# Kernel tuning notes

Hardware: AMD Instinct MI355X
Metric: run time of the kernel (lower is better)

## Reference

```python
import jax, jax.numpy as jnp
import numpy as np

D_IN = 1024
D_OUT = 1024
N, S = 4, 2048

def setup_inputs() -> dict:
    key = jax.random.key(0)
    kv, kk, kq, k1, k2, k3 = jax.random.split(key, 6)
    return {
        "v": jax.random.normal(kv, (N, S, D_IN), dtype=jnp.float32),
        "k": jax.random.normal(kk, (N, S, D_IN), dtype=jnp.float32),
        "q": jax.random.normal(kq, (N, S, D_IN), dtype=jnp.float32),
        "WV": jax.random.normal(k1, (D_OUT, D_IN), dtype=jnp.float32),
        "WQ": jax.random.normal(k2, (D_OUT, D_IN), dtype=jnp.float32),
        "WK": jax.random.normal(k3, (D_OUT, D_IN), dtype=jnp.float32),
    }

def reference(v, k, q, WV, WQ, WK) -> jnp.ndarray:
    # projections: x @ W.T  -> [N, S, D_OUT]
    wv = jnp.einsum('nsw,ow->nso', v, WV)
    wk = jnp.einsum('nsw,ow->nso', k, WK)
    wq = jnp.einsum('nsw,ow->nso', q, WQ)
    # scores [N, Sq, Sk]; NOTE: softmax over axis=1 (query axis, matching torch dim=1),
    # then post-hoc division by input_shape[0] AFTER softmax (faithful to source).
    scores = jnp.einsum('nqo,nko->nqk', wq, wk)
    wqk = jax.nn.softmax(scores, axis=1) / jnp.float32(D_IN)
    return jnp.einsum('nqk,nko->nqo', wqk, wv)
```

## Files before the change

### kernel.cpp

```cpp
#include <hip/hip_runtime.h>
#include <math.h>


typedef _Float16 f16;
typedef _Float16 f16x8 __attribute__((ext_vector_type(8)));
typedef _Float16 f16x4 __attribute__((ext_vector_type(4)));
typedef float f32x4 __attribute__((ext_vector_type(4)));

enum StageMode { SM_PLANES2, SM_PLANES1 };
enum EpiMode   { EPI_F32, EPI_SPLIT, EPI_F16T };

#define GLL_PITCH 32

__device__ __forceinline__ void gll16(const f16* g, f16* l) {
    __builtin_amdgcn_global_load_lds(
        (const __attribute__((address_space(1))) void*)g,
        (__attribute__((address_space(3))) void*)l, 16, 0, 0);
}

__device__ __forceinline__ void stage_gll_plane(const f16* __restrict__ gplane,
                                                f16* __restrict__ lds,
                                                long rowBase, int ld, int k0,
                                                int wave, int lane)
{
#pragma unroll
    for (int i = 0; i < 2; i++) {
        int slotBase = (wave * 2 + i) * 64;
        int t = slotBase + lane;
        int r = t >> 2;
        int c = (t & 3) ^ ((r >> 1) & 3);
        const f16* g = gplane + (rowBase + r) * (long)ld + k0 + c * 8;
        gll16(g, lds + (long)slotBase * 8);
    }
}

__device__ __forceinline__ int frag_off_gll(int row, int g) {
    return row * GLL_PITCH + ((g ^ ((row >> 1) & 3)) << 3);
}

template<StageMode SA, StageMode SB, EpiMode EP, int GROUPM, bool STATS>
__global__ __launch_bounds__(256, 4)
void mfma_gemm(const f16* __restrict__ Ahi, const f16* __restrict__ Alo,
               const f16* __restrict__ Bhi, const f16* __restrict__ Blo,
               float* __restrict__ pmOut, float* __restrict__ psOut,
               void* __restrict__ C0, void* __restrict__ C1,
               int M, int Nc, int K, int lda, int ldb, int ldc,
               long batchA, long batchB, long batchC,
               float epiScale, int tsShift)
{
    constexpr bool TRIPLE = (SA == SM_PLANES2);
    constexpr int PLANE_SZ = 128 * GLL_PITCH;

    int bx, by;
    if constexpr (GROUPM > 0) {
        int gx = gridDim.x;
        int lin = blockIdx.y * gx + blockIdx.x;
        int nig = GROUPM * gx;
        int gid = lin / nig;
        int rem = lin - gid * nig;
        by = gid * GROUPM + (rem % GROUPM);
        bx = rem / GROUPM;
    } else {
        bx = blockIdx.x;
        by = blockIdx.y;
    }
    const int n0 = bx * 128;
    const int m0 = by * 128;
    const long z = blockIdx.z;

    const long aOfs = z * batchA, bOfs = z * batchB, cOfs = z * batchC;

    __shared__ __align__(16) f16 As_hi[PLANE_SZ];
    __shared__ __align__(16) f16 Bs_hi[PLANE_SZ];
    __shared__ __align__(16) f16 As_lo[TRIPLE ? PLANE_SZ : 8];
    __shared__ __align__(16) f16 Bs_lo[TRIPLE ? PLANE_SZ : 8];

    const int tid  = threadIdx.x;
    const int lane = tid & 63;
    const int wave = tid >> 6;
    const int wr = (wave >> 1) * 64;
    const int wc = (wave & 1) * 64;
    const int fm = lane & 15;
    const int fg = lane >> 4;

    f32x4 acc[4][4];
#pragma unroll
    for (int i = 0; i < 4; i++)
#pragma unroll
        for (int j = 0; j < 4; j++) acc[i][j] = (f32x4){0.f, 0.f, 0.f, 0.f};

    int roA[4], roB[4];
#pragma unroll
    for (int i = 0; i < 4; i++) {
        roA[i] = frag_off_gll(wr + i * 16 + fm, fg);
        roB[i] = frag_off_gll(wc + i * 16 + fm, fg);
    }

    for (int k0 = 0; k0 < K; k0 += 32) {
        stage_gll_plane(Ahi + aOfs, As_hi, m0, lda, k0, wave, lane);
        stage_gll_plane(Bhi + bOfs, Bs_hi, n0, ldb, k0, wave, lane);
        if constexpr (TRIPLE) {
            stage_gll_plane(Alo + aOfs, As_lo, m0, lda, k0, wave, lane);
            stage_gll_plane(Blo + bOfs, Bs_lo, n0, ldb, k0, wave, lane);
        }
        __syncthreads();

        f16x8 ah[4], bh[4], al[4], bl[4];
#pragma unroll
        for (int i = 0; i < 4; i++) {
            ah[i] = *(const f16x8*)&As_hi[roA[i]];
            bh[i] = *(const f16x8*)&Bs_hi[roB[i]];
            if constexpr (TRIPLE) {
                al[i] = *(const f16x8*)&As_lo[roA[i]];
                bl[i] = *(const f16x8*)&Bs_lo[roB[i]];
            }
        }
#pragma unroll
        for (int i = 0; i < 4; i++) {
#pragma unroll
            for (int j = 0; j < 4; j++) {
                acc[i][j] = __builtin_amdgcn_mfma_f32_16x16x32_f16(ah[i], bh[j], acc[i][j], 0, 0, 0);
                if constexpr (TRIPLE) {
                    acc[i][j] = __builtin_amdgcn_mfma_f32_16x16x32_f16(ah[i], bl[j], acc[i][j], 0, 0, 0);
                    acc[i][j] = __builtin_amdgcn_mfma_f32_16x16x32_f16(al[i], bh[j], acc[i][j], 0, 0, 0);
                }
            }
        }
        __syncthreads();
    }

    const int cr = fg * 4;
    const int cn = fm;
#pragma unroll
    for (int i = 0; i < 4; i++) {
#pragma unroll
        for (int j = 0; j < 4; j++) {
#pragma unroll
            for (int r = 0; r < 4; r++) {
                long mg = m0 + wr + i * 16 + cr + r;
                long ng = n0 + wc + j * 16 + cn;
                float val = acc[i][j][r] * epiScale;
                if constexpr (EP == EPI_F32) {
                    ((float*)C0)[cOfs + mg * ldc + ng] = val;
                } else if constexpr (EP == EPI_SPLIT) {
                    f16 h = (f16)val;
                    ((f16*)C0)[cOfs + mg * ldc + ng] = h;
                    ((f16*)C1)[cOfs + mg * ldc + ng] = (f16)(val - (float)h);
                } else {
                    long TS = 1L << tsShift;
                    long nb = mg >> tsShift;
                    long s  = mg & (TS - 1);
                    long addr = nb * ((long)Nc << tsShift) + ng * TS + s;
                    ((f16*)C0)[addr] = (f16)val;
                }
            }
        }
    }
}

template<EpiMode EP, bool STATS, bool XCDMAP, bool DUAL>
__global__ __launch_bounds__(512, 2)
void big_gemm(const f16* __restrict__ Ahi, const f16* __restrict__ Alo,
              const f16* __restrict__ Bhi, const f16* __restrict__ Blo,
              const f16* __restrict__ A2hi, const f16* __restrict__ A2lo,
              const f16* __restrict__ B2hi, const f16* __restrict__ B2lo,
              float* __restrict__ pmOut, float* __restrict__ psOut,
              void* __restrict__ C0, void* __restrict__ C1,
              void* __restrict__ C20, void* __restrict__ C21,
              int M, int Nc, int K, int lda, int ldb, int ldc,
              long batchA, long batchB, long batchC, int msplitTiles)
{
    constexpr int PLANE = 256 * GLL_PITCH;

    __shared__ __align__(16) f16 As_hi[2][PLANE];
    __shared__ __align__(16) f16 As_lo[2][PLANE];
    __shared__ __align__(16) f16 Bs_hi[2][PLANE];
    __shared__ __align__(16) f16 Bs_lo[2][PLANE];

    const int tid  = threadIdx.x;
    const int lane = tid & 63;
    const int wave = tid >> 6;
    const int rw   = wave >> 2;
    const int cw   = wave & 3;
    const int wrM  = rw * 128;
    const int wrN  = cw * 64;
    const int fm   = lane & 15;
    const int fg   = lane >> 4;

    int bxn, byn, zn;
    if constexpr (XCDMAP) {
        const int Lid = (int)(blockIdx.z * 64 + blockIdx.y * 8 + blockIdx.x);
        const int xcd = Lid & 7;
        const int sct = Lid >> 3;
        bxn = sct & 7;
        const int idxp = xcd * 4 + (sct >> 3);
        byn = idxp & 7;
        zn  = idxp >> 3;
    } else {
        bxn = blockIdx.x;
        byn = blockIdx.y;
        zn  = blockIdx.z;
    }

    const f16* pAhi = Ahi; const f16* pAlo = Alo;
    const f16* pBhi = Bhi; const f16* pBlo = Blo;
    void* pC0 = C0; void* pC1 = C1;
    int mTile = byn;
    if constexpr (DUAL) {
        if (byn >= msplitTiles) {
            pAhi = A2hi; pAlo = A2lo; pBhi = B2hi; pBlo = B2lo;
            pC0 = C20; pC1 = C21;
            mTile = byn - msplitTiles;
        }
    }

    const int n0 = bxn * 256;
    const int m0 = mTile * 256;
    const long z = zn;
    const long aOfs = z * batchA, bOfs = z * batchB, cOfs = z * batchC;

    int slotBase[2], srcA[2], srcB[2];
#pragma unroll
    for (int i = 0; i < 2; i++) {
        int sb = (wave * 2 + i) * 64;
        int t  = sb + lane;
        int r  = t >> 2;
        int c  = (t & 3) ^ ((r >> 1) & 3);
        slotBase[i] = sb * 8;
        srcA[i] = (m0 + r) * lda + c * 8;
        srcB[i] = (n0 + r) * ldb + c * 8;
    }

#define SC_STAGE(buf, k0) do {                                               \
    _Pragma("unroll")                                                        \
    for (int s_ = 0; s_ < 2; s_++) {                                         \
        gll16(pAhi + aOfs + srcA[s_] + (k0), &As_hi[buf][slotBase[s_]]);     \
        gll16(pAlo + aOfs + srcA[s_] + (k0), &As_lo[buf][slotBase[s_]]);     \
        gll16(pBhi + bOfs + srcB[s_] + (k0), &Bs_hi[buf][slotBase[s_]]);     \
        gll16(pBlo + bOfs + srcB[s_] + (k0), &Bs_lo[buf][slotBase[s_]]);     \
    } } while (0)

    f32x4 acc[8][4];
#pragma unroll
    for (int i = 0; i < 8; i++)
#pragma unroll
        for (int j = 0; j < 4; j++) acc[i][j] = (f32x4){0.f, 0.f, 0.f, 0.f};

    int roA[8], roB[4];
#pragma unroll
    for (int i = 0; i < 8; i++) roA[i] = frag_off_gll(wrM + i * 16 + fm, fg);
#pragma unroll
    for (int j = 0; j < 4; j++) roB[j] = frag_off_gll(wrN + j * 16 + fm, fg);

    const int NT = K >> 5;
    SC_STAGE(0, 0);
    SC_STAGE(1, 32);

    for (int t = 0; t < NT; t++) {
        const int cur = t & 1;
        if (t == 0) {
            asm volatile("s_waitcnt vmcnt(8)" ::: "memory");
        } else {
            asm volatile("s_waitcnt vmcnt(0)" ::: "memory");
        }
        __builtin_amdgcn_sched_barrier(0);
        __builtin_amdgcn_s_barrier();
        __builtin_amdgcn_sched_barrier(0);

        if (t >= 1 && t + 1 < NT) SC_STAGE(cur ^ 1, (t + 1) * 32);
        __builtin_amdgcn_sched_barrier(0);

        f16x8 bh[4], a0h[4];
#pragma unroll
        for (int j = 0; j < 4; j++) bh[j] = *(const f16x8*)&Bs_hi[cur][roB[j]];
#pragma unroll
        for (int i = 0; i < 4; i++) a0h[i] = *(const f16x8*)&As_hi[cur][roA[i]];
        __builtin_amdgcn_sched_barrier(0);
        f16x8 bl[4], a0l[4];
#pragma unroll
        for (int j = 0; j < 4; j++) bl[j] = *(const f16x8*)&Bs_lo[cur][roB[j]];
#pragma unroll
        for (int i = 0; i < 4; i++) a0l[i] = *(const f16x8*)&As_lo[cur][roA[i]];
        __builtin_amdgcn_sched_barrier(0);

        __builtin_amdgcn_s_setprio(1);
#pragma unroll
        for (int i = 0; i < 4; i++)
#pragma unroll
            for (int j = 0; j < 4; j++)
                acc[i][j] = __builtin_amdgcn_mfma_f32_16x16x32_f16(a0h[i], bh[j], acc[i][j], 0, 0, 0);
        __builtin_amdgcn_s_setprio(0);
        __builtin_amdgcn_sched_barrier(0);

        f16x8 a1h[4], a1l[4];
#pragma unroll
        for (int i = 0; i < 4; i++) {
            a1h[i] = *(const f16x8*)&As_hi[cur][roA[4 + i]];
            a1l[i] = *(const f16x8*)&As_lo[cur][roA[4 + i]];
        }
        __builtin_amdgcn_sched_barrier(0);

        __builtin_amdgcn_s_setprio(1);
#pragma unroll
        for (int i = 0; i < 4; i++)
#pragma unroll
            for (int j = 0; j < 4; j++)
                acc[i][j] = __builtin_amdgcn_mfma_f32_16x16x32_f16(a0h[i], bl[j], acc[i][j], 0, 0, 0);
#pragma unroll
        for (int i = 0; i < 4; i++)
#pragma unroll
            for (int j = 0; j < 4; j++)
                acc[i][j] = __builtin_amdgcn_mfma_f32_16x16x32_f16(a0l[i], bh[j], acc[i][j], 0, 0, 0);
        __builtin_amdgcn_s_setprio(0);
        __builtin_amdgcn_sched_barrier(0);

        __builtin_amdgcn_s_setprio(1);
#pragma unroll
        for (int i = 0; i < 4; i++)
#pragma unroll
            for (int j = 0; j < 4; j++)
                acc[4 + i][j] = __builtin_amdgcn_mfma_f32_16x16x32_f16(a1h[i], bh[j], acc[4 + i][j], 0, 0, 0);
#pragma unroll
        for (int i = 0; i < 4; i++)
#pragma unroll
            for (int j = 0; j < 4; j++)
                acc[4 + i][j] = __builtin_amdgcn_mfma_f32_16x16x32_f16(a1h[i], bl[j], acc[4 + i][j], 0, 0, 0);
#pragma unroll
        for (int i = 0; i < 4; i++)
#pragma unroll
            for (int j = 0; j < 4; j++)
                acc[4 + i][j] = __builtin_amdgcn_mfma_f32_16x16x32_f16(a1l[i], bh[j], acc[4 + i][j], 0, 0, 0);
        __builtin_amdgcn_s_setprio(0);
    }
#undef SC_STAGE

    const int cr = fg * 4;
#pragma unroll
    for (int i = 0; i < 8; i++) {
#pragma unroll
        for (int j = 0; j < 4; j++) {
#pragma unroll
            for (int r = 0; r < 4; r++) {
                long mg = m0 + wrM + i * 16 + cr + r;
                long ng = n0 + wrN + j * 16 + fm;
                float val = acc[i][j][r];
                if constexpr (EP == EPI_F32) {
                    ((float*)pC0)[cOfs + mg * (long)ldc + ng] = val;
                } else {
                    f16 h = (f16)val;
                    ((f16*)pC0)[cOfs + mg * (long)ldc + ng] = h;
                    ((f16*)pC1)[cOfs + mg * (long)ldc + ng] = (f16)(val - (float)h);
                }
            }
        }
    }

    if constexpr (STATS) {
        __shared__ float stM[2][256];
        __shared__ float stS[2][256];
#pragma unroll
        for (int j = 0; j < 4; j++) {
            float mj = -3.402823466e38f;
#pragma unroll
            for (int i = 0; i < 8; i++)
#pragma unroll
                for (int r = 0; r < 4; r++) mj = fmaxf(mj, acc[i][j][r]);
            float sj = 0.f;
#pragma unroll
            for (int i = 0; i < 8; i++)
#pragma unroll
                for (int r = 0; r < 4; r++) sj += __expf(acc[i][j][r] - mj);
#pragma unroll
            for (int mask = 16; mask <= 32; mask <<= 1) {
                float mo = __shfl_xor(mj, mask, 64);
                float so = __shfl_xor(sj, mask, 64);
                float mn = fmaxf(mj, mo);
                sj = sj * __expf(mj - mn) + so * __expf(mo - mn);
                mj = mn;
            }
            if (fg == 0) {
                stM[rw][wrN + j * 16 + fm] = mj;
                stS[rw][wrN + j * 16 + fm] = sj;
            }
        }
        __syncthreads();
        if (tid < 256) {
            float ma = stM[0][tid], mb = stM[1][tid];
            float Mc = fmaxf(ma, mb);
            float Sv = stS[0][tid] * __expf(ma - Mc) + stS[1][tid] * __expf(mb - Mc);
            long o = ((long)z * (M >> 8) + byn) * (long)Nc + (long)bxn * 256 + tid;
            pmOut[o] = Mc;
            psOut[o] = Sv;
        }
    }
}

__global__ __launch_bounds__(256)
void split_all_kernel(const float* __restrict__ q, const float* __restrict__ k,
                      const float* __restrict__ v, const float* __restrict__ WQ,
                      const float* __restrict__ WK, const float* __restrict__ WV,
                      f16* __restrict__ ws, long NSD, long DD)
{
    const long QB = NSD / 2048;
    const long WB = DD / 2048;
    const long b = blockIdx.x;
    f16* Wb = ws + 5 * NSD;

    const float* src;
    f16* hi;
    f16* lo = nullptr;
    long base;
    if (b < QB)               { src = q;  base = b * 2048;                 hi = ws;           lo = ws + NSD;   }
    else if (b < 2 * QB)      { src = k;  base = (b - QB) * 2048;          hi = ws + 2 * NSD; lo = ws + 3 * NSD; }
    else if (b < 3 * QB)      { src = v;  base = (b - 2 * QB) * 2048;      hi = ws + 4 * NSD; }
    else if (b < 3 * QB + WB) { src = WQ; base = (b - 3 * QB) * 2048;      hi = Wb;           lo = Wb + DD;    }
    else if (b < 3 * QB + 2 * WB) { src = WK; base = (b - 3 * QB - WB) * 2048; hi = Wb + 2 * DD; lo = Wb + 3 * DD; }
    else                      { src = WV; base = (b - 3 * QB - 2 * WB) * 2048; hi = Wb + 4 * DD; }

    long i = base + (long)threadIdx.x * 8;
    float4 x0 = *(const float4*)&src[i];
    float4 x1 = *(const float4*)&src[i + 4];
    float xs[8] = {x0.x, x0.y, x0.z, x0.w, x1.x, x1.y, x1.z, x1.w};
    f16x8 h, l;
#pragma unroll
    for (int e = 0; e < 8; e++) {
        f16 hh = (f16)xs[e];
        h[e] = hh;
        l[e] = (f16)(xs[e] - (float)hh);
    }
    *(f16x8*)&hi[i] = h;
    if (lo) *(f16x8*)&lo[i] = l;
}

__global__ __launch_bounds__(256)
void pmat_kernel(const float* __restrict__ Sc, const float* __restrict__ pm,
                 const float* __restrict__ ps, f16* __restrict__ Phi, int S)
{
    const int n = blockIdx.z;
    const int kk = blockIdx.x * 1024 + threadIdx.x * 4;
    const float* Sn = Sc + (long)n * S * S;
    f16* ph = Phi + (long)n * S * S;

    float M4[4], R4[4];
#pragma unroll
    for (int c = 0; c < 4; c++) {
        const int col = kk + c;
        float pmv[8];
        float M = -INFINITY;
#pragma unroll
        for (int i = 0; i < 8; i++) {
            pmv[i] = pm[((long)n * 8 + i) * S + col];
            M = fmaxf(M, pmv[i]);
        }
        float Ssum = 0.f;
#pragma unroll
        for (int i = 0; i < 8; i++)
            Ssum += ps[((long)n * 8 + i) * S + col] * __expf(pmv[i] - M);
        M4[c] = M;
        R4[c] = 1.0f / Ssum;
    }

    const int q0 = blockIdx.y * 32;
    for (int qi = 0; qi < 32; qi++) {
        long idx = (long)(q0 + qi) * S + kk;
        float4 x = *(const float4*)&Sn[idx];
        f16x4 p;
        p[0] = (f16)(__expf(x.x - M4[0]) * R4[0]);
        p[1] = (f16)(__expf(x.y - M4[1]) * R4[1]);
        p[2] = (f16)(__expf(x.z - M4[2]) * R4[2]);
        p[3] = (f16)(__expf(x.w - M4[3]) * R4[3]);
        *(f16x4*)&ph[idx] = p;
    }
}

extern "C" void kernel_launch(void* const* d_in, const int* in_sizes, int n_in,
                              void* d_out, int out_size, void* d_ws, size_t ws_size,
                              hipStream_t stream)
{
    const float* v  = (const float*)d_in[0];
    const float* k  = (const float*)d_in[1];
    const float* q  = (const float*)d_in[2];
    const float* WV = (const float*)d_in[3];
    const float* WQ = (const float*)d_in[4];
    const float* WK = (const float*)d_in[5];
    float* out = (float*)d_out;

    const int N = 4, S = 2048, D = 1024;
    const long NSD = (long)N * S * D;
    const long DD  = (long)D * D;

    f16* ws = (f16*)d_ws;
    f16* q_hi = ws;
    f16* q_lo = ws + NSD;
    f16* k_hi = ws + 2 * NSD;
    f16* k_lo = ws + 3 * NSD;
    f16* v_hi = ws + 4 * NSD;
    f16* Wb   = ws + 5 * NSD;
    f16* WQ_hi = Wb,          *WQ_lo = Wb + DD;
    f16* WK_hi = Wb + 2 * DD, *WK_lo = Wb + 3 * DD;
    f16* WV_hi = Wb + 4 * DD;
    f16* wq_hi = ws + 5 * NSD + 5 * DD;
    f16* wq_lo = wq_hi + NSD;
    f16* wk_hi = wq_hi + 2 * NSD;
    f16* wk_lo = wq_hi + 3 * NSD;
    f16* wvT_hi = ws;
    float* Sc   = (float*)(ws + NSD);
    f16* P_hi   = wq_hi;
    float* pm    = (float*)(ws + 9 * NSD + 5 * DD);
    float* ps    = pm + (long)N * 8 * S;

    dim3 blk(256);

    {
        long nblocks = 3 * (NSD / 2048) + 3 * (DD / 2048);
        split_all_kernel<<<dim3((unsigned)nblocks), blk, 0, stream>>>(
            q, k, v, WQ, WK, WV, ws, NSD, DD);
    }

    {
        dim3 g(D / 256, (2 * N * S) / 256, 1);
        big_gemm<EPI_SPLIT, false, false, true><<<g, dim3(512), 0, stream>>>(
            q_hi, q_lo, WQ_hi, WQ_lo,
            k_hi, k_lo, WK_hi, WK_lo,
            nullptr, nullptr,
            wq_hi, wq_lo, wk_hi, wk_lo,
            2 * N * S, D, D, D, D, D, 0, 0, 0, (N * S) / 256 );
    }
    {
        dim3 g(D / 128, (N * S) / 128, 1);
        mfma_gemm<SM_PLANES1, SM_PLANES1, EPI_F16T, 4, false><<<g, blk, 0, stream>>>(
            v_hi, nullptr, WV_hi, nullptr, nullptr, nullptr, wvT_hi, nullptr,
            N * S, D, D, D, D, 0, 0, 0, 0, 1.0f, 11 );
    }
    {
        dim3 g(S / 256, S / 256, N);
        big_gemm<EPI_F32, true, true, false><<<g, dim3(512), 0, stream>>>(
            wq_hi, wq_lo, wk_hi, wk_lo,
            nullptr, nullptr, nullptr, nullptr,
            pm, ps, Sc, nullptr, nullptr, nullptr,
            S, S, D, D, D, S, (long)S * D, (long)S * D, (long)S * S, 1 << 30);
    }
    {
        dim3 g(S / 1024, S / 32, N);
        pmat_kernel<<<g, blk, 0, stream>>>(Sc, pm, ps, P_hi, S);
    }
    {
        dim3 g(D / 128, S / 128, N);
        mfma_gemm<SM_PLANES1, SM_PLANES1, EPI_F32, 4, false><<<g, blk, 0, stream>>>(
            P_hi, nullptr, wvT_hi, nullptr, nullptr, nullptr, out, nullptr,
            S, D, S, S, S, D, (long)S * S, (long)S * D, (long)S * D, 1.0f / (float)D, 0);
    }
}
```

Measured before the change: 438.7 us.

## Route single-plane GEMMs through the double-buffered 256x256 big_gemm kernel

Removes the simple 128x128 single-buffered mfma_gemm kernel. The V projection and the final P·V GEMM now run on big_gemm, which gains a TRIPLE template flag so it can skip the low-precision planes, plus the F16T transposed epilogue and an epilogue scale. It also adds an XCD-aware block remapping mode for the dual Q/K projection. The aim is to get larger tiles, double-buffered async loads and more data reuse for the fp16-only GEMMs. The cost is fewer blocks per launch (for example 128 for the P·V GEMM), which may lower occupancy, and the remap assumes a fixed grid shape.

```diff
diff --git a/kernel.cpp b/kernel.cpp
--- a/kernel.cpp
+++ b/kernel.cpp
@@ -7,8 +7,7 @@
 typedef _Float16 f16x4 __attribute__((ext_vector_type(4)));
 typedef float f32x4 __attribute__((ext_vector_type(4)));
 
-enum StageMode { SM_PLANES2, SM_PLANES1 };
-enum EpiMode   { EPI_F32, EPI_SPLIT, EPI_F16T };
+enum EpiMode { EPI_F32, EPI_SPLIT, EPI_F16T };
 
 #define GLL_PITCH 32
 
@@ -18,147 +17,11 @@
         (__attribute__((address_space(3))) void*)l, 16, 0, 0);
 }
 
-__device__ __forceinline__ void stage_gll_plane(const f16* __restrict__ gplane,
-                                                f16* __restrict__ lds,
-                                                long rowBase, int ld, int k0,
-                                                int wave, int lane)
-{
-#pragma unroll
-    for (int i = 0; i < 2; i++) {
-        int slotBase = (wave * 2 + i) * 64;
-        int t = slotBase + lane;
-        int r = t >> 2;
-        int c = (t & 3) ^ ((r >> 1) & 3);
-        const f16* g = gplane + (rowBase + r) * (long)ld + k0 + c * 8;
-        gll16(g, lds + (long)slotBase * 8);
-    }
-}
-
 __device__ __forceinline__ int frag_off_gll(int row, int g) {
     return row * GLL_PITCH + ((g ^ ((row >> 1) & 3)) << 3);
 }
 
-template<StageMode SA, StageMode SB, EpiMode EP, int GROUPM, bool STATS>
-__global__ __launch_bounds__(256, 4)
-void mfma_gemm(const f16* __restrict__ Ahi, const f16* __restrict__ Alo,
-               const f16* __restrict__ Bhi, const f16* __restrict__ Blo,
-               float* __restrict__ pmOut, float* __restrict__ psOut,
-               void* __restrict__ C0, void* __restrict__ C1,
-               int M, int Nc, int K, int lda, int ldb, int ldc,
-               long batchA, long batchB, long batchC,
-               float epiScale, int tsShift)
-{
-    constexpr bool TRIPLE = (SA == SM_PLANES2);
-    constexpr int PLANE_SZ = 128 * GLL_PITCH;
-
-    int bx, by;
-    if constexpr (GROUPM > 0) {
-        int gx = gridDim.x;
-        int lin = blockIdx.y * gx + blockIdx.x;
-        int nig = GROUPM * gx;
-        int gid = lin / nig;
-        int rem = lin - gid * nig;
-        by = gid * GROUPM + (rem % GROUPM);
-        bx = rem / GROUPM;
-    } else {
-        bx = blockIdx.x;
-        by = blockIdx.y;
-    }
-    const int n0 = bx * 128;
-    const int m0 = by * 128;
-    const long z = blockIdx.z;
-
-    const long aOfs = z * batchA, bOfs = z * batchB, cOfs = z * batchC;
-
-    __shared__ __align__(16) f16 As_hi[PLANE_SZ];
-    __shared__ __align__(16) f16 Bs_hi[PLANE_SZ];
-    __shared__ __align__(16) f16 As_lo[TRIPLE ? PLANE_SZ : 8];
-    __shared__ __align__(16) f16 Bs_lo[TRIPLE ? PLANE_SZ : 8];
-
-    const int tid  = threadIdx.x;
-    const int lane = tid & 63;
-    const int wave = tid >> 6;
-    const int wr = (wave >> 1) * 64;
-    const int wc = (wave & 1) * 64;
-    const int fm = lane & 15;
-    const int fg = lane >> 4;
-
-    f32x4 acc[4][4];
-#pragma unroll
-    for (int i = 0; i < 4; i++)
-#pragma unroll
-        for (int j = 0; j < 4; j++) acc[i][j] = (f32x4){0.f, 0.f, 0.f, 0.f};
-
-    int roA[4], roB[4];
-#pragma unroll
-    for (int i = 0; i < 4; i++) {
-        roA[i] = frag_off_gll(wr + i * 16 + fm, fg);
-        roB[i] = frag_off_gll(wc + i * 16 + fm, fg);
-    }
-
-    for (int k0 = 0; k0 < K; k0 += 32) {
-        stage_gll_plane(Ahi + aOfs, As_hi, m0, lda, k0, wave, lane);
-        stage_gll_plane(Bhi + bOfs, Bs_hi, n0, ldb, k0, wave, lane);
-        if constexpr (TRIPLE) {
-            stage_gll_plane(Alo + aOfs, As_lo, m0, lda, k0, wave, lane);
-            stage_gll_plane(Blo + bOfs, Bs_lo, n0, ldb, k0, wave, lane);
-        }
-        __syncthreads();
-
-        f16x8 ah[4], bh[4], al[4], bl[4];
-#pragma unroll
-        for (int i = 0; i < 4; i++) {
-            ah[i] = *(const f16x8*)&As_hi[roA[i]];
-            bh[i] = *(const f16x8*)&Bs_hi[roB[i]];
-            if constexpr (TRIPLE) {
-                al[i] = *(const f16x8*)&As_lo[roA[i]];
-                bl[i] = *(const f16x8*)&Bs_lo[roB[i]];
-            }
-        }
-#pragma unroll
-        for (int i = 0; i < 4; i++) {
-#pragma unroll
-            for (int j = 0; j < 4; j++) {
-                acc[i][j] = __builtin_amdgcn_mfma_f32_16x16x32_f16(ah[i], bh[j], acc[i][j], 0, 0, 0);
-                if constexpr (TRIPLE) {
-                    acc[i][j] = __builtin_amdgcn_mfma_f32_16x16x32_f16(ah[i], bl[j], acc[i][j], 0, 0, 0);
-                    acc[i][j] = __builtin_amdgcn_mfma_f32_16x16x32_f16(al[i], bh[j], acc[i][j], 0, 0, 0);
-                }
-            }
-        }
-        __syncthreads();
-    }
-
-    const int cr = fg * 4;
-    const int cn = fm;
-#pragma unroll
-    for (int i = 0; i < 4; i++) {
-#pragma unroll
-        for (int j = 0; j < 4; j++) {
-#pragma unroll
-            for (int r = 0; r < 4; r++) {
-                long mg = m0 + wr + i * 16 + cr + r;
-                long ng = n0 + wc + j * 16 + cn;
-                float val = acc[i][j][r] * epiScale;
-                if constexpr (EP == EPI_F32) {
-                    ((float*)C0)[cOfs + mg * ldc + ng] = val;
-                } else if constexpr (EP == EPI_SPLIT) {
-                    f16 h = (f16)val;
-                    ((f16*)C0)[cOfs + mg * ldc + ng] = h;
-                    ((f16*)C1)[cOfs + mg * ldc + ng] = (f16)(val - (float)h);
-                } else {
-                    long TS = 1L << tsShift;
-                    long nb = mg >> tsShift;
-                    long s  = mg & (TS - 1);
-                    long addr = nb * ((long)Nc << tsShift) + ng * TS + s;
-                    ((f16*)C0)[addr] = (f16)val;
-                }
-            }
-        }
-    }
-}
-
-template<EpiMode EP, bool STATS, bool XCDMAP, bool DUAL>
+template<EpiMode EP, bool STATS, int XCDMODE, bool DUAL, bool TRIPLE>
 __global__ __launch_bounds__(512, 2)
 void big_gemm(const f16* __restrict__ Ahi, const f16* __restrict__ Alo,
               const f16* __restrict__ Bhi, const f16* __restrict__ Blo,
@@ -168,14 +31,15 @@
               void* __restrict__ C0, void* __restrict__ C1,
               void* __restrict__ C20, void* __restrict__ C21,
               int M, int Nc, int K, int lda, int ldb, int ldc,
-              long batchA, long batchB, long batchC, int msplitTiles)
+              long batchA, long batchB, long batchC, int msplitTiles,
+              float epiScale, int tsShift)
 {
     constexpr int PLANE = 256 * GLL_PITCH;
 
     __shared__ __align__(16) f16 As_hi[2][PLANE];
-    __shared__ __align__(16) f16 As_lo[2][PLANE];
     __shared__ __align__(16) f16 Bs_hi[2][PLANE];
-    __shared__ __align__(16) f16 Bs_lo[2][PLANE];
+    __shared__ __align__(16) f16 As_lo[2][TRIPLE ? PLANE : 8];
+    __shared__ __align__(16) f16 Bs_lo[2][TRIPLE ? PLANE : 8];
 
     const int tid  = threadIdx.x;
     const int lane = tid & 63;
@@ -188,7 +52,7 @@
     const int fg   = lane >> 4;
 
     int bxn, byn, zn;
-    if constexpr (XCDMAP) {
+    if constexpr (XCDMODE == 1) {
         const int Lid = (int)(blockIdx.z * 64 + blockIdx.y * 8 + blockIdx.x);
         const int xcd = Lid & 7;
         const int sct = Lid >> 3;
@@ -196,6 +60,13 @@
         const int idxp = xcd * 4 + (sct >> 3);
         byn = idxp & 7;
         zn  = idxp >> 3;
+    } else if constexpr (XCDMODE == 2) {
+        const int Lid = (int)(blockIdx.y * 4 + blockIdx.x);
+        const int xcd = Lid & 7;
+        const int sct = Lid >> 3;
+        bxn = sct & 3;
+        byn = xcd * 8 + (sct >> 2);
+        zn  = 0;
     } else {
         bxn = blockIdx.x;
         byn = blockIdx.y;
@@ -231,13 +102,15 @@
         srcB[i] = (n0 + r) * ldb + c * 8;
     }
 
-#define SC_STAGE(buf, k0) do {                                               \
-    _Pragma("unroll")                                                        \
-    for (int s_ = 0; s_ < 2; s_++) {                                         \
-        gll16(pAhi + aOfs + srcA[s_] + (k0), &As_hi[buf][slotBase[s_]]);     \
-        gll16(pAlo + aOfs + srcA[s_] + (k0), &As_lo[buf][slotBase[s_]]);     \
-        gll16(pBhi + bOfs + srcB[s_] + (k0), &Bs_hi[buf][slotBase[s_]]);     \
-        gll16(pBlo + bOfs + srcB[s_] + (k0), &Bs_lo[buf][slotBase[s_]]);     \
+#define SC_STAGE(buf, k0) do {                                                   \
+    _Pragma("unroll")                                                            \
+    for (int s_ = 0; s_ < 2; s_++) {                                             \
+        gll16(pAhi + aOfs + srcA[s_] + (k0), &As_hi[buf][slotBase[s_]]);         \
+        gll16(pBhi + bOfs + srcB[s_] + (k0), &Bs_hi[buf][slotBase[s_]]);         \
+        if constexpr (TRIPLE) {                                                  \
+            gll16(pAlo + aOfs + srcA[s_] + (k0), &As_lo[buf][slotBase[s_]]);     \
+            gll16(pBlo + bOfs + srcB[s_] + (k0), &Bs_lo[buf][slotBase[s_]]);     \
+        }                                                                        \
     } } while (0)
 
     f32x4 acc[8][4];
@@ -259,7 +132,8 @@
     for (int t = 0; t < NT; t++) {
         const int cur = t & 1;
         if (t == 0) {
-            asm volatile("s_waitcnt vmcnt(8)" ::: "memory");
+            if constexpr (TRIPLE) asm volatile("s_waitcnt vmcnt(8)" ::: "memory");
+            else                  asm volatile("s_waitcnt vmcnt(4)" ::: "memory");
         } else {
             asm volatile("s_waitcnt vmcnt(0)" ::: "memory");
         }
@@ -277,11 +151,13 @@
         for (int i = 0; i < 4; i++) a0h[i] = *(const f16x8*)&As_hi[cur][roA[i]];
         __builtin_amdgcn_sched_barrier(0);
         f16x8 bl[4], a0l[4];
-#pragma unroll
-        for (int j = 0; j < 4; j++) bl[j] = *(const f16x8*)&Bs_lo[cur][roB[j]];
-#pragma unroll
-        for (int i = 0; i < 4; i++) a0l[i] = *(const f16x8*)&As_lo[cur][roA[i]];
-        __builtin_amdgcn_sched_barrier(0);
+        if constexpr (TRIPLE) {
+#pragma unroll
+            for (int j = 0; j < 4; j++) bl[j] = *(const f16x8*)&Bs_lo[cur][roB[j]];
+#pragma unroll
+            for (int i = 0; i < 4; i++) a0l[i] = *(const f16x8*)&As_lo[cur][roA[i]];
+            __builtin_amdgcn_sched_barrier(0);
+        }
 
         __builtin_amdgcn_s_setprio(1);
 #pragma unroll
@@ -296,23 +172,25 @@
 #pragma unroll
         for (int i = 0; i < 4; i++) {
             a1h[i] = *(const f16x8*)&As_hi[cur][roA[4 + i]];
-            a1l[i] = *(const f16x8*)&As_lo[cur][roA[4 + i]];
-        }
-        __builtin_amdgcn_sched_barrier(0);
-
-        __builtin_amdgcn_s_setprio(1);
-#pragma unroll
-        for (int i = 0; i < 4; i++)
-#pragma unroll
-            for (int j = 0; j < 4; j++)
-                acc[i][j] = __builtin_amdgcn_mfma_f32_16x16x32_f16(a0h[i], bl[j], acc[i][j], 0, 0, 0);
-#pragma unroll
-        for (int i = 0; i < 4; i++)
-#pragma unroll
-            for (int j = 0; j < 4; j++)
-                acc[i][j] = __builtin_amdgcn_mfma_f32_16x16x32_f16(a0l[i], bh[j], acc[i][j], 0, 0, 0);
-        __builtin_amdgcn_s_setprio(0);
-        __builtin_amdgcn_sched_barrier(0);
+            if constexpr (TRIPLE) a1l[i] = *(const f16x8*)&As_lo[cur][roA[4 + i]];
+        }
+        __builtin_amdgcn_sched_barrier(0);
+
+        if constexpr (TRIPLE) {
+            __builtin_amdgcn_s_setprio(1);
+#pragma unroll
+            for (int i = 0; i < 4; i++)
+#pragma unroll
+                for (int j = 0; j < 4; j++)
+                    acc[i][j] = __builtin_amdgcn_mfma_f32_16x16x32_f16(a0h[i], bl[j], acc[i][j], 0, 0, 0);
+#pragma unroll
+            for (int i = 0; i < 4; i++)
+#pragma unroll
+                for (int j = 0; j < 4; j++)
+                    acc[i][j] = __builtin_amdgcn_mfma_f32_16x16x32_f16(a0l[i], bh[j], acc[i][j], 0, 0, 0);
+            __builtin_amdgcn_s_setprio(0);
+            __builtin_amdgcn_sched_barrier(0);
+        }
 
         __builtin_amdgcn_s_setprio(1);
 #pragma unroll
@@ -320,16 +198,18 @@
 #pragma unroll
             for (int j = 0; j < 4; j++)
                 acc[4 + i][j] = __builtin_amdgcn_mfma_f32_16x16x32_f16(a1h[i], bh[j], acc[4 + i][j], 0, 0, 0);
-#pragma unroll
-        for (int i = 0; i < 4; i++)
-#pragma unroll
-            for (int j = 0; j < 4; j++)
-                acc[4 + i][j] = __builtin_amdgcn_mfma_f32_16x16x32_f16(a1h[i], bl[j], acc[4 + i][j], 0, 0, 0);
-#pragma unroll
-        for (int i = 0; i < 4; i++)
-#pragma unroll
-            for (int j = 0; j < 4; j++)
-                acc[4 + i][j] = __builtin_amdgcn_mfma_f32_16x16x32_f16(a1l[i], bh[j], acc[4 + i][j], 0, 0, 0);
+        if constexpr (TRIPLE) {
+#pragma unroll
+            for (int i = 0; i < 4; i++)
+#pragma unroll
+                for (int j = 0; j < 4; j++)
+                    acc[4 + i][j] = __builtin_amdgcn_mfma_f32_16x16x32_f16(a1h[i], bl[j], acc[4 + i][j], 0, 0, 0);
+#pragma unroll
+            for (int i = 0; i < 4; i++)
+#pragma unroll
+                for (int j = 0; j < 4; j++)
+                    acc[4 + i][j] = __builtin_amdgcn_mfma_f32_16x16x32_f16(a1l[i], bh[j], acc[4 + i][j], 0, 0, 0);
+        }
         __builtin_amdgcn_s_setprio(0);
     }
 #undef SC_STAGE
@@ -343,13 +223,19 @@
             for (int r = 0; r < 4; r++) {
                 long mg = m0 + wrM + i * 16 + cr + r;
                 long ng = n0 + wrN + j * 16 + fm;
-                float val = acc[i][j][r];
+                float val = acc[i][j][r] * epiScale;
                 if constexpr (EP == EPI_F32) {
                     ((float*)pC0)[cOfs + mg * (long)ldc + ng] = val;
-                } else {
+                } else if constexpr (EP == EPI_SPLIT) {
                     f16 h = (f16)val;
                     ((f16*)pC0)[cOfs + mg * (long)ldc + ng] = h;
                     ((f16*)pC1)[cOfs + mg * (long)ldc + ng] = (f16)(val - (float)h);
+                } else {
+                    long TS = 1L << tsShift;
+                    long nb = mg >> tsShift;
+                    long s  = mg & (TS - 1);
+                    long addr = nb * ((long)Nc << tsShift) + ng * TS + s;
+                    ((f16*)pC0)[addr] = (f16)val;
                 }
             }
         }
@@ -519,35 +405,42 @@
 
     {
         dim3 g(D / 256, (2 * N * S) / 256, 1);
-        big_gemm<EPI_SPLIT, false, false, true><<<g, dim3(512), 0, stream>>>(
+        big_gemm<EPI_SPLIT, false, 2, true, true><<<g, dim3(512), 0, stream>>>(
             q_hi, q_lo, WQ_hi, WQ_lo,
             k_hi, k_lo, WK_hi, WK_lo,
             nullptr, nullptr,
             wq_hi, wq_lo, wk_hi, wk_lo,
-            2 * N * S, D, D, D, D, D, 0, 0, 0, (N * S) / 256 );
-    }
-    {
-        dim3 g(D / 128, (N * S) / 128, 1);
-        mfma_gemm<SM_PLANES1, SM_PLANES1, EPI_F16T, 4, false><<<g, blk, 0, stream>>>(
-            v_hi, nullptr, WV_hi, nullptr, nullptr, nullptr, wvT_hi, nullptr,
-            N * S, D, D, D, D, 0, 0, 0, 0, 1.0f, 11 );
+            2 * N * S, D, D, D, D, D, 0, 0, 0, (N * S) / 256 , 1.0f, 0);
+    }
+    {
+        dim3 g(D / 256, (N * S) / 256, 1);
+        big_gemm<EPI_F16T, false, 0, false, false><<<g, dim3(512), 0, stream>>>(
+            v_hi, nullptr, WV_hi, nullptr,
+            nullptr, nullptr, nullptr, nullptr,
+            nullptr, nullptr,
+            wvT_hi, nullptr, nullptr, nullptr,
+            N * S, D, D, D, D, 0, 0, 0, 0, 1 << 30, 1.0f, 11 );
     }
     {
         dim3 g(S / 256, S / 256, N);
-        big_gemm<EPI_F32, true, true, false><<<g, dim3(512), 0, stream>>>(
+        big_gemm<EPI_F32, true, 1, false, true><<<g, dim3(512), 0, stream>>>(
             wq_hi, wq_lo, wk_hi, wk_lo,
             nullptr, nullptr, nullptr, nullptr,
             pm, ps, Sc, nullptr, nullptr, nullptr,
-            S, S, D, D, D, S, (long)S * D, (long)S * D, (long)S * S, 1 << 30);
+            S, S, D, D, D, S, (long)S * D, (long)S * D, (long)S * S, 1 << 30, 1.0f, 0);
     }
     {
         dim3 g(S / 1024, S / 32, N);
         pmat_kernel<<<g, blk, 0, stream>>>(Sc, pm, ps, P_hi, S);
     }
     {
-        dim3 g(D / 128, S / 128, N);
-        mfma_gemm<SM_PLANES1, SM_PLANES1, EPI_F32, 4, false><<<g, blk, 0, stream>>>(
-            P_hi, nullptr, wvT_hi, nullptr, nullptr, nullptr, out, nullptr,
-            S, D, S, S, S, D, (long)S * S, (long)S * D, (long)S * D, 1.0f / (float)D, 0);
-    }
-}
+        dim3 g(D / 256, S / 256, N);
+        big_gemm<EPI_F32, false, 0, false, false><<<g, dim3(512), 0, stream>>>(
+            P_hi, nullptr, wvT_hi, nullptr,
+            nullptr, nullptr, nullptr, nullptr,
+            nullptr, nullptr,
+            out, nullptr, nullptr, nullptr,
+            S, D, S, S, S, D, (long)S * S, (long)S * D, (long)S * D, 1 << 30,
+            1.0f / (float)D, 0);
+    }
+}
```

New measurement: 496.7 us. +13.2%, slower.

## Fuse tile-local exp into scores GEMM epilogue, store f16 scores, remap projection blocks

Applied to the files above, without the earlier changes.

The scores GEMM now finishes its per-tile column statistics first, then writes exp(score - tileMax) as f16 instead of raw f32 scores. The softmax kernel becomes a cheap in-place rescale of those f16 values by a per-column weight built from the tile and global maxima. This halves the score-matrix traffic and moves the exponentials into the GEMM epilogue. It also adds an XCD-aware block remap for the fused Q/K projection GEMM and a template switch to drop the lo-plane loads and MFMAs (all current launches keep them), at the cost of an extra f16 rounding of the unnormalised probabilities.

```diff
diff --git a/kernel.cpp b/kernel.cpp
--- a/kernel.cpp
+++ b/kernel.cpp
@@ -158,7 +158,7 @@
     }
 }
 
-template<EpiMode EP, bool STATS, bool XCDMAP, bool DUAL>
+template<EpiMode EP, bool STATS, int XCDMODE, bool DUAL, bool TRIPLE>
 __global__ __launch_bounds__(512, 2)
 void big_gemm(const f16* __restrict__ Ahi, const f16* __restrict__ Alo,
               const f16* __restrict__ Bhi, const f16* __restrict__ Blo,
@@ -173,9 +173,9 @@
     constexpr int PLANE = 256 * GLL_PITCH;
 
     __shared__ __align__(16) f16 As_hi[2][PLANE];
-    __shared__ __align__(16) f16 As_lo[2][PLANE];
     __shared__ __align__(16) f16 Bs_hi[2][PLANE];
-    __shared__ __align__(16) f16 Bs_lo[2][PLANE];
+    __shared__ __align__(16) f16 As_lo[2][TRIPLE ? PLANE : 8];
+    __shared__ __align__(16) f16 Bs_lo[2][TRIPLE ? PLANE : 8];
 
     const int tid  = threadIdx.x;
     const int lane = tid & 63;
@@ -188,7 +188,7 @@
     const int fg   = lane >> 4;
 
     int bxn, byn, zn;
-    if constexpr (XCDMAP) {
+    if constexpr (XCDMODE == 1) {
         const int Lid = (int)(blockIdx.z * 64 + blockIdx.y * 8 + blockIdx.x);
         const int xcd = Lid & 7;
         const int sct = Lid >> 3;
@@ -196,6 +196,13 @@
         const int idxp = xcd * 4 + (sct >> 3);
         byn = idxp & 7;
         zn  = idxp >> 3;
+    } else if constexpr (XCDMODE == 2) {
+        const int Lid = (int)(blockIdx.y * 4 + blockIdx.x);
+        const int xcd = Lid & 7;
+        const int sct = Lid >> 3;
+        bxn = sct & 3;
+        byn = xcd * 8 + (sct >> 2);
+        zn  = 0;
     } else {
         bxn = blockIdx.x;
         byn = blockIdx.y;
@@ -231,13 +238,15 @@
         srcB[i] = (n0 + r) * ldb + c * 8;
     }
 
-#define SC_STAGE(buf, k0) do {                                               \
-    _Pragma("unroll")                                                        \
-    for (int s_ = 0; s_ < 2; s_++) {                                         \
-        gll16(pAhi + aOfs + srcA[s_] + (k0), &As_hi[buf][slotBase[s_]]);     \
-        gll16(pAlo + aOfs + srcA[s_] + (k0), &As_lo[buf][slotBase[s_]]);     \
-        gll16(pBhi + bOfs + srcB[s_] + (k0), &Bs_hi[buf][slotBase[s_]]);     \
-        gll16(pBlo + bOfs + srcB[s_] + (k0), &Bs_lo[buf][slotBase[s_]]);     \
+#define SC_STAGE(buf, k0) do {                                                   \
+    _Pragma("unroll")                                                            \
+    for (int s_ = 0; s_ < 2; s_++) {                                             \
+        gll16(pAhi + aOfs + srcA[s_] + (k0), &As_hi[buf][slotBase[s_]]);         \
+        gll16(pBhi + bOfs + srcB[s_] + (k0), &Bs_hi[buf][slotBase[s_]]);         \
+        if constexpr (TRIPLE) {                                                  \
+            gll16(pAlo + aOfs + srcA[s_] + (k0), &As_lo[buf][slotBase[s_]]);     \
+            gll16(pBlo + bOfs + srcB[s_] + (k0), &Bs_lo[buf][slotBase[s_]]);     \
+        }                                                                        \
     } } while (0)
 
     f32x4 acc[8][4];
@@ -259,7 +268,8 @@
     for (int t = 0; t < NT; t++) {
         const int cur = t & 1;
         if (t == 0) {
-            asm volatile("s_waitcnt vmcnt(8)" ::: "memory");
+            if constexpr (TRIPLE) asm volatile("s_waitcnt vmcnt(8)" ::: "memory");
+            else                  asm volatile("s_waitcnt vmcnt(4)" ::: "memory");
         } else {
             asm volatile("s_waitcnt vmcnt(0)" ::: "memory");
         }
@@ -277,11 +287,13 @@
         for (int i = 0; i < 4; i++) a0h[i] = *(const f16x8*)&As_hi[cur][roA[i]];
         __builtin_amdgcn_sched_barrier(0);
         f16x8 bl[4], a0l[4];
-#pragma unroll
-        for (int j = 0; j < 4; j++) bl[j] = *(const f16x8*)&Bs_lo[cur][roB[j]];
-#pragma unroll
-        for (int i = 0; i < 4; i++) a0l[i] = *(const f16x8*)&As_lo[cur][roA[i]];
-        __builtin_amdgcn_sched_barrier(0);
+        if constexpr (TRIPLE) {
+#pragma unroll
+            for (int j = 0; j < 4; j++) bl[j] = *(const f16x8*)&Bs_lo[cur][roB[j]];
+#pragma unroll
+            for (int i = 0; i < 4; i++) a0l[i] = *(const f16x8*)&As_lo[cur][roA[i]];
+            __builtin_amdgcn_sched_barrier(0);
+        }
 
         __builtin_amdgcn_s_setprio(1);
 #pragma unroll
@@ -296,23 +308,25 @@
 #pragma unroll
         for (int i = 0; i < 4; i++) {
             a1h[i] = *(const f16x8*)&As_hi[cur][roA[4 + i]];
-            a1l[i] = *(const f16x8*)&As_lo[cur][roA[4 + i]];
+            if constexpr (TRIPLE) a1l[i] = *(const f16x8*)&As_lo[cur][roA[4 + i]];
         }
         __builtin_amdgcn_sched_barrier(0);
 
-        __builtin_amdgcn_s_setprio(1);
-#pragma unroll
-        for (int i = 0; i < 4; i++)
-#pragma unroll
-            for (int j = 0; j < 4; j++)
-                acc[i][j] = __builtin_amdgcn_mfma_f32_16x16x32_f16(a0h[i], bl[j], acc[i][j], 0, 0, 0);
-#pragma unroll
-        for (int i = 0; i < 4; i++)
-#pragma unroll
-            for (int j = 0; j < 4; j++)
-                acc[i][j] = __builtin_amdgcn_mfma_f32_16x16x32_f16(a0l[i], bh[j], acc[i][j], 0, 0, 0);
-        __builtin_amdgcn_s_setprio(0);
-        __builtin_amdgcn_sched_barrier(0);
+        if constexpr (TRIPLE) {
+            __builtin_amdgcn_s_setprio(1);
+#pragma unroll
+            for (int i = 0; i < 4; i++)
+#pragma unroll
+                for (int j = 0; j < 4; j++)
+                    acc[i][j] = __builtin_amdgcn_mfma_f32_16x16x32_f16(a0h[i], bl[j], acc[i][j], 0, 0, 0);
+#pragma unroll
+            for (int i = 0; i < 4; i++)
+#pragma unroll
+                for (int j = 0; j < 4; j++)
+                    acc[i][j] = __builtin_amdgcn_mfma_f32_16x16x32_f16(a0l[i], bh[j], acc[i][j], 0, 0, 0);
+            __builtin_amdgcn_s_setprio(0);
+            __builtin_amdgcn_sched_barrier(0);
+        }
 
         __builtin_amdgcn_s_setprio(1);
 #pragma unroll
@@ -320,40 +334,23 @@
 #pragma unroll
             for (int j = 0; j < 4; j++)
                 acc[4 + i][j] = __builtin_amdgcn_mfma_f32_16x16x32_f16(a1h[i], bh[j], acc[4 + i][j], 0, 0, 0);
-#pragma unroll
-        for (int i = 0; i < 4; i++)
-#pragma unroll
-            for (int j = 0; j < 4; j++)
-                acc[4 + i][j] = __builtin_amdgcn_mfma_f32_16x16x32_f16(a1h[i], bl[j], acc[4 + i][j], 0, 0, 0);
-#pragma unroll
-        for (int i = 0; i < 4; i++)
-#pragma unroll
-            for (int j = 0; j < 4; j++)
-                acc[4 + i][j] = __builtin_amdgcn_mfma_f32_16x16x32_f16(a1l[i], bh[j], acc[4 + i][j], 0, 0, 0);
+        if constexpr (TRIPLE) {
+#pragma unroll
+            for (int i = 0; i < 4; i++)
+#pragma unroll
+                for (int j = 0; j < 4; j++)
+                    acc[4 + i][j] = __builtin_amdgcn_mfma_f32_16x16x32_f16(a1h[i], bl[j], acc[4 + i][j], 0, 0, 0);
+#pragma unroll
+            for (int i = 0; i < 4; i++)
+#pragma unroll
+                for (int j = 0; j < 4; j++)
+                    acc[4 + i][j] = __builtin_amdgcn_mfma_f32_16x16x32_f16(a1l[i], bh[j], acc[4 + i][j], 0, 0, 0);
+        }
         __builtin_amdgcn_s_setprio(0);
     }
 #undef SC_STAGE
 
     const int cr = fg * 4;
-#pragma unroll
-    for (int i = 0; i < 8; i++) {
-#pragma unroll
-        for (int j = 0; j < 4; j++) {
-#pragma unroll
-            for (int r = 0; r < 4; r++) {
-                long mg = m0 + wrM + i * 16 + cr + r;
-                long ng = n0 + wrN + j * 16 + fm;
-                float val = acc[i][j][r];
-                if constexpr (EP == EPI_F32) {
-                    ((float*)pC0)[cOfs + mg * (long)ldc + ng] = val;
-                } else {
-                    f16 h = (f16)val;
-                    ((f16*)pC0)[cOfs + mg * (long)ldc + ng] = h;
-                    ((f16*)pC1)[cOfs + mg * (long)ldc + ng] = (f16)(val - (float)h);
-                }
-            }
-        }
-    }
 
     if constexpr (STATS) {
         __shared__ float stM[2][256];
@@ -391,6 +388,43 @@
             long o = ((long)z * (M >> 8) + byn) * (long)Nc + (long)bxn * 256 + tid;
             pmOut[o] = Mc;
             psOut[o] = Sv;
+            stM[0][tid] = Mc;
+        }
+        __syncthreads();
+
+#pragma unroll
+        for (int j = 0; j < 4; j++) {
+            const float Mc = stM[0][wrN + j * 16 + fm];
+#pragma unroll
+            for (int i = 0; i < 8; i++) {
+#pragma unroll
+                for (int r = 0; r < 4; r++) {
+                    long mg = m0 + wrM + i * 16 + cr + r;
+                    long ng = n0 + wrN + j * 16 + fm;
+                    ((f16*)pC0)[cOfs + mg * (long)ldc + ng] =
+                        (f16)__expf(acc[i][j][r] - Mc);
+                }
+            }
+        }
+    } else {
+#pragma unroll
+        for (int i = 0; i < 8; i++) {
+#pragma unroll
+            for (int j = 0; j < 4; j++) {
+#pragma unroll
+                for (int r = 0; r < 4; r++) {
+                    long mg = m0 + wrM + i * 16 + cr + r;
+                    long ng = n0 + wrN + j * 16 + fm;
+                    float val = acc[i][j][r];
+                    if constexpr (EP == EPI_F32) {
+                        ((float*)pC0)[cOfs + mg * (long)ldc + ng] = val;
+                    } else {
+                        f16 h = (f16)val;
+                        ((f16*)pC0)[cOfs + mg * (long)ldc + ng] = h;
+                        ((f16*)pC1)[cOfs + mg * (long)ldc + ng] = (f16)(val - (float)h);
+                    }
+                }
+            }
         }
     }
 }
@@ -433,15 +467,16 @@
 }
 
 __global__ __launch_bounds__(256)
-void pmat_kernel(const float* __restrict__ Sc, const float* __restrict__ pm,
-                 const float* __restrict__ ps, f16* __restrict__ Phi, int S)
+void pmat_kernel(f16* __restrict__ P, const float* __restrict__ pm,
+                 const float* __restrict__ ps, int S)
 {
     const int n = blockIdx.z;
     const int kk = blockIdx.x * 1024 + threadIdx.x * 4;
-    const float* Sn = Sc + (long)n * S * S;
-    f16* ph = Phi + (long)n * S * S;
-
-    float M4[4], R4[4];
+    const int q0 = blockIdx.y * 32;
+    const int tile = q0 >> 8;
+    f16* Pn = P + (long)n * S * S;
+
+    float w4[4];
 #pragma unroll
     for (int c = 0; c < 4; c++) {
         const int col = kk + c;
@@ -456,20 +491,16 @@
 #pragma unroll
         for (int i = 0; i < 8; i++)
             Ssum += ps[((long)n * 8 + i) * S + col] * __expf(pmv[i] - M);
-        M4[c] = M;
-        R4[c] = 1.0f / Ssum;
-    }
-
-    const int q0 = blockIdx.y * 32;
+        w4[c] = __expf(pmv[tile] - M) / Ssum;
+    }
+
     for (int qi = 0; qi < 32; qi++) {
         long idx = (long)(q0 + qi) * S + kk;
-        float4 x = *(const float4*)&Sn[idx];
+        f16x4 ph = *(const f16x4*)&Pn[idx];
         f16x4 p;
-        p[0] = (f16)(__expf(x.x - M4[0]) * R4[0]);
-        p[1] = (f16)(__expf(x.y - M4[1]) * R4[1]);
-        p[2] = (f16)(__expf(x.z - M4[2]) * R4[2]);
-        p[3] = (f16)(__expf(x.w - M4[3]) * R4[3]);
-        *(f16x4*)&ph[idx] = p;
+#pragma unroll
+        for (int e = 0; e < 4; e++) p[e] = (f16)((float)ph[e] * w4[e]);
+        *(f16x4*)&Pn[idx] = p;
     }
 }
 
@@ -504,8 +535,7 @@
     f16* wk_hi = wq_hi + 2 * NSD;
     f16* wk_lo = wq_hi + 3 * NSD;
     f16* wvT_hi = ws;
-    float* Sc   = (float*)(ws + NSD);
-    f16* P_hi   = wq_hi;
+    f16* Sc16   = ws + NSD;
     float* pm    = (float*)(ws + 9 * NSD + 5 * DD);
     float* ps    = pm + (long)N * 8 * S;
 
@@ -519,7 +549,7 @@
 
     {
         dim3 g(D / 256, (2 * N * S) / 256, 1);
-        big_gemm<EPI_SPLIT, false, false, true><<<g, dim3(512), 0, stream>>>(
+        big_gemm<EPI_SPLIT, false, 2, true, true><<<g, dim3(512), 0, stream>>>(
             q_hi, q_lo, WQ_hi, WQ_lo,
             k_hi, k_lo, WK_hi, WK_lo,
             nullptr, nullptr,
@@ -534,20 +564,20 @@
     }
     {
         dim3 g(S / 256, S / 256, N);
-        big_gemm<EPI_F32, true, true, false><<<g, dim3(512), 0, stream>>>(
+        big_gemm<EPI_F32, true, 1, false, true><<<g, dim3(512), 0, stream>>>(
             wq_hi, wq_lo, wk_hi, wk_lo,
             nullptr, nullptr, nullptr, nullptr,
-            pm, ps, Sc, nullptr, nullptr, nullptr,
+            pm, ps, Sc16, nullptr, nullptr, nullptr,
             S, S, D, D, D, S, (long)S * D, (long)S * D, (long)S * S, 1 << 30);
     }
     {
         dim3 g(S / 1024, S / 32, N);
-        pmat_kernel<<<g, blk, 0, stream>>>(Sc, pm, ps, P_hi, S);
+        pmat_kernel<<<g, blk, 0, stream>>>(Sc16, pm, ps, S);
     }
     {
         dim3 g(D / 128, S / 128, N);
         mfma_gemm<SM_PLANES1, SM_PLANES1, EPI_F32, 4, false><<<g, blk, 0, stream>>>(
-            P_hi, nullptr, wvT_hi, nullptr, nullptr, nullptr, out, nullptr,
+            Sc16, nullptr, wvT_hi, nullptr, nullptr, nullptr, out, nullptr,
             S, D, S, S, S, D, (long)S * S, (long)S * D, (long)S * D, 1.0f / (float)D, 0);
     }
 }
```

Measured after the change: 444.1 us. Within noise of the previous version (+1.2%).
